# Optimization experiments

Measured on AMD Instinct MI355X. Metric: run time of the kernel, lower is better.

## Reference

```python
import jax, jax.numpy as jnp
import numpy as np

B, T, LD, HD, NH, NL = 8, 16, 256, 512, 8, 6
N = 65           # num_patches + 1 tokens per frame from encoder
AED = 64         # action_embed_dim
NDA = 11         # num_discrete_actions
MLP = 4 * HD


def _ln(x, g, b, eps=1e-5):
    m = jnp.mean(x, -1, keepdims=True)
    v = jnp.mean((x - m) ** 2, -1, keepdims=True)
    return (x - m) / jnp.sqrt(v + eps) * g + b


def setup_inputs() -> dict:
    key = jax.random.key(0)
    ks = iter(jax.random.split(key, 48))
    def nrm(shape):
        return jax.random.normal(next(ks), shape, jnp.float32) * 0.02
    inp = {
        'z_sequence': jax.random.normal(next(ks), (B, T, N, LD), jnp.float32),
        'continuous_actions': jax.random.normal(next(ks), (B, T, 2), jnp.float32),
        'discrete_actions': jax.random.randint(next(ks), (B, T), 0, NDA),
        'w_de': nrm((NDA, AED)),
        'w_cp': nrm((2, AED)), 'b_cp': jnp.zeros((AED,), jnp.float32),
        'w_ap': nrm((2 * AED, HD)), 'b_ap': jnp.zeros((HD,), jnp.float32),
        'w_tp': nrm((LD, HD)), 'b_tp': jnp.zeros((HD,), jnp.float32),
        'w_te': nrm((64, HD)),
        'ln1_g': jnp.ones((NL, HD), jnp.float32), 'ln1_b': jnp.zeros((NL, HD), jnp.float32),
        'wq': nrm((NL, HD, HD)), 'bq': jnp.zeros((NL, HD), jnp.float32),
        'wk': nrm((NL, HD, HD)), 'bk': jnp.zeros((NL, HD), jnp.float32),
        'wv': nrm((NL, HD, HD)), 'bv': jnp.zeros((NL, HD), jnp.float32),
        'wo': nrm((NL, HD, HD)), 'bo': jnp.zeros((NL, HD), jnp.float32),
        'ln2_g': jnp.ones((NL, HD), jnp.float32), 'ln2_b': jnp.zeros((NL, HD), jnp.float32),
        'w1': nrm((NL, HD, MLP)), 'b1': jnp.zeros((NL, MLP), jnp.float32),
        'w2': nrm((NL, MLP, HD)), 'b2': jnp.zeros((NL, HD), jnp.float32),
        'norm_g': jnp.ones((HD,), jnp.float32), 'norm_b': jnp.zeros((HD,), jnp.float32),
        'w_out': nrm((HD, LD)), 'b_out': jnp.zeros((LD,), jnp.float32),
        'residual_weight': jnp.float32(0.5),
    }
    return inp


def reference(z_sequence, continuous_actions, discrete_actions,
              w_de, w_cp, b_cp, w_ap, b_ap, w_tp, b_tp, w_te,
              ln1_g, ln1_b, wq, bq, wk, bk, wv, bv, wo, bo,
              ln2_g, ln2_b, w1, b1, w2, b2,
              norm_g, norm_b, w_out, b_out, residual_weight):
    Bq, Tq, Nq, Dq = z_sequence.shape
    hd = HD // NH
    scale = hd ** -0.5
    # --- per-timestep action + patch token embedding (vectorized over T) ---
    de = w_de[discrete_actions]                          # (B,T,AED)
    ce = continuous_actions @ w_cp + b_cp                # (B,T,AED)
    ac = jnp.concatenate([de, ce], -1)                   # (B,T,2*AED)
    at = (ac @ w_ap + b_ap)[:, :, None, :]               # (B,T,1,HD) action token
    pt = z_sequence @ w_tp + b_tp                        # (B,T,N,HD)
    te = w_te[:Tq][None, :, None, :]                     # (1,T,1,HD) time embedding
    x = jnp.concatenate([at + te, pt + te], axis=2)      # (B,T,1+N,HD) interleaved
    S = Tq * (Nq + 1)
    x = x.reshape(Bq, S, HD)
    # --- block-causal mask: True = cannot attend ---
    ts = jnp.repeat(jnp.arange(Tq), Nq + 1)
    mask = ts[None, :] > ts[:, None]                     # (S,S)

    def body(h, p):
        g1, be1, Wq, Bq_, Wk, Bk_, Wv, Bv_, Wo, Bo_, g2, be2, W1, B1, W2, B2 = p
        y = _ln(h, g1, be1)
        q = (y @ Wq + Bq_).reshape(Bq, S, NH, hd)
        k = (y @ Wk + Bk_).reshape(Bq, S, NH, hd)
        v = (y @ Wv + Bv_).reshape(Bq, S, NH, hd)
        sc = jnp.einsum('bqhd,bkhd->bhqk', q, k) * scale
        sc = jnp.where(mask[None, None], -jnp.inf, sc)
        a = jax.nn.softmax(sc, axis=-1)
        o = jnp.einsum('bhqk,bkhd->bqhd', a, v).reshape(Bq, S, HD)
        h = h + o @ Wo + Bo_
        y = _ln(h, g2, be2)
        h = h + jax.nn.gelu(y @ W1 + B1, approximate=False) @ W2 + B2
        return h, None

    x, _ = jax.lax.scan(body, x, (ln1_g, ln1_b, wq, bq, wk, bk, wv, bv, wo, bo,
                                  ln2_g, ln2_b, w1, b1, w2, b2))
    x = _ln(x, norm_g, norm_b)
    patch_out = x.reshape(Bq, Tq, Nq + 1, HD)[:, :, 1:, :] @ w_out + b_out
    alpha = jax.nn.sigmoid(residual_weight)
    return z_sequence + alpha * patch_out
```

## Files before the change

### kernel.cpp

```cpp
#include <hip/hip_runtime.h>
#include <hip/hip_bf16.h>
#include <cmath>

typedef __attribute__((ext_vector_type(8)))  __bf16 bf16x8;
typedef __attribute__((ext_vector_type(4)))  float  f32x4;
typedef __attribute__((ext_vector_type(16))) float  f32x16;
typedef const __attribute__((address_space(1))) void* as1cv;
typedef __attribute__((address_space(3))) void*       as3v;

static constexpr int BB = 8, TT = 16, NN = 65, LD = 256, HD = 512, NH = 8, NL = 6;
static constexpr int SS    = TT * (NN + 1);
static constexpr int ROWS  = BB * SS;
static constexpr int PROWS = BB * TT * NN;
static constexpr int MLPD  = 2048;

__global__ void transpose_cast(const float* __restrict__ in, __bf16* __restrict__ out,
                               int R, int C, size_t ibs, size_t obs)
{
  __shared__ float t[32][33];
  in  += ibs * blockIdx.z;
  out += obs * blockIdx.z;
  int bx = blockIdx.x * 32, by = blockIdx.y * 32;
  #pragma unroll
  for (int i = threadIdx.y; i < 32; i += 8)
    t[i][threadIdx.x] = in[(size_t)(by + i) * C + bx + threadIdx.x];
  __syncthreads();
  #pragma unroll
  for (int i = threadIdx.y; i < 32; i += 8)
    out[(size_t)(bx + i) * R + by + threadIdx.x] = (__bf16)t[threadIdx.x][i];
}

__global__ __launch_bounds__(256) void cast_bf16(const float* __restrict__ in,
                                                 __bf16* __restrict__ out)
{
  int i = (blockIdx.x * 256 + threadIdx.x) * 8;
  float4 a = *(const float4*)(in + i);
  float4 b = *(const float4*)(in + i + 4);
  bf16x8 o;
  o[0]=(__bf16)a.x; o[1]=(__bf16)a.y; o[2]=(__bf16)a.z; o[3]=(__bf16)a.w;
  o[4]=(__bf16)b.x; o[5]=(__bf16)b.y; o[6]=(__bf16)b.z; o[7]=(__bf16)b.w;
  *(bf16x8*)(out + i) = o;
}

__global__ void build_bqkv(const float* __restrict__ bq, const float* __restrict__ bk,
                           const float* __restrict__ bv, float* __restrict__ out)
{
  int i = blockIdx.x * 256 + threadIdx.x;
  int L = i / 1536, c = i % 1536;
  float v = (c < 512) ? bq[L*512 + c] : (c < 1024 ? bk[L*512 + c - 512] : bv[L*512 + c - 1024]);
  out[i] = v;
}

template<int FLAGS>
__global__ __launch_bounds__(256)
void gemm_bt(const __bf16* __restrict__ A, const __bf16* __restrict__ Bt,
             const float* __restrict__ bias, const float* __restrict__ resid,
             float* __restrict__ outF, __bf16* __restrict__ outB, __bf16* __restrict__ outB2,
             int M, int N, int K)
{
  __shared__ __bf16 As[64 * 64];
  __shared__ __bf16 Bs[128 * 64];
  const int tid = threadIdx.x;
  const int lane = tid & 63, w = tid >> 6;
  const int g = lane >> 4, cl = lane & 15;
  const int wr = w >> 1, wc = w & 1;
  const int gx = gridDim.x, nwg = gx * gridDim.y;
  const int orig = blockIdx.y * gx + blockIdx.x;
  const int q8 = nwg >> 3, r8 = nwg & 7;
  const int xcd = orig & 7, off = orig >> 3;
  const int tile = (xcd < r8 ? xcd * (q8 + 1) : r8 * (q8 + 1) + (xcd - r8) * q8) + off;
  const int tm = (tile / gx) * 64, tn = (tile % gx) * 128;

  f32x4 acc[2][4];
  const f32x4 zero4 = {0.f, 0.f, 0.f, 0.f};
  #pragma unroll
  for (int m = 0; m < 2; m++)
    #pragma unroll
    for (int n = 0; n < 4; n++) acc[m][n] = zero4;

  const int nk = K >> 6;
  for (int kt = 0; kt < nk; ++kt) {
    __syncthreads();
    const __bf16* Ag = A  + (size_t)tm * K + kt * 64;
    const __bf16* Bg = Bt + (size_t)tn * K + kt * 64;
    #pragma unroll
    for (int p = 0; p < 2; p++) {
      int c = p * 256 + tid;
      int row = c >> 3, j = c & 7;
      int jj = j ^ (row & 7);
      const __bf16* sa = Ag + (size_t)row * K + jj * 8;
      __builtin_amdgcn_global_load_lds((as1cv)sa, (as3v)&As[(p * 4 + w) * 512], 16, 0, 0);
    }
    #pragma unroll
    for (int p = 0; p < 4; p++) {
      int c = p * 256 + tid;
      int row = c >> 3, j = c & 7;
      int jj = j ^ (row & 7);
      const __bf16* sb = Bg + (size_t)row * K + jj * 8;
      __builtin_amdgcn_global_load_lds((as1cv)sb, (as3v)&Bs[(p * 4 + w) * 512], 16, 0, 0);
    }
    __syncthreads();
    #pragma unroll
    for (int kk = 0; kk < 2; kk++) {
      bf16x8 af[2], bfr[4];
      #pragma unroll
      for (int m = 0; m < 2; m++) {
        int row = wr * 32 + m * 16 + cl;
        af[m] = *(const bf16x8*)&As[row * 64 + ((kk * 4 + g) ^ (row & 7)) * 8];
      }
      #pragma unroll
      for (int n = 0; n < 4; n++) {
        int row = wc * 64 + n * 16 + cl;
        bfr[n] = *(const bf16x8*)&Bs[row * 64 + ((kk * 4 + g) ^ (row & 7)) * 8];
      }
      #pragma unroll
      for (int m = 0; m < 2; m++)
        #pragma unroll
        for (int n = 0; n < 4; n++)
          acc[m][n] = __builtin_amdgcn_mfma_f32_16x16x32_bf16(af[m], bfr[n], acc[m][n], 0, 0, 0);
    }
  }
  float bv[4];
  #pragma unroll
  for (int n = 0; n < 4; n++) bv[n] = bias[tn + wc * 64 + n * 16 + cl];
  #pragma unroll
  for (int m = 0; m < 2; m++) {
    int Rb = tm + wr * 32 + m * 16 + g * 4;
    #pragma unroll
    for (int i = 0; i < 4; i++) {
      int R = Rb + i;
      #pragma unroll
      for (int n = 0; n < 4; n++) {
        int C = tn + wc * 64 + n * 16 + cl;
        float v = acc[m][n][i] + bv[n];
        if (FLAGS & 1) v = 0.5f * v * (1.f + erff(v * 0.70710678118f));
        if (FLAGS & 2) v += resid[(size_t)R * N + C];
        if (FLAGS & 8) outF[(size_t)R * N + C] = v;
        if (FLAGS & 4) outB[(size_t)R * N + C] = (__bf16)v;
        if (FLAGS & 32) {
          if (C < 1024) {
            outB[(size_t)R * 1024 + C] = (__bf16)v;
          } else {
            int bb2 = R / SS, s2 = R % SS;
            int cc = C - 1024, hh = cc >> 6, dd = cc & 63;
            outB2[((size_t)((bb2 * NH + hh) * 64 + dd)) * SS + s2] = (__bf16)v;
          }
        }
      }
    }
  }
}

template<int FLAGS>
__global__ __launch_bounds__(256)
void gemm_n64(const __bf16* __restrict__ A, const __bf16* __restrict__ Bt,
              const float* __restrict__ bias, const float* __restrict__ resid,
              float* __restrict__ outF, __bf16* __restrict__ outB,
              int M, int N, int K)
{
  __shared__ __bf16 As[64 * 64];
  __shared__ __bf16 Bs[64 * 64];
  const int tid = threadIdx.x;
  const int lane = tid & 63, w = tid >> 6;
  const int g = lane >> 4, cl = lane & 15;
  const int wr = w >> 1, wc = w & 1;
  const int gx = gridDim.x, nwg = gx * gridDim.y;
  const int orig = blockIdx.y * gx + blockIdx.x;
  const int q8 = nwg >> 3, r8 = nwg & 7;
  const int xcd = orig & 7, off = orig >> 3;
  const int tile = (xcd < r8 ? xcd * (q8 + 1) : r8 * (q8 + 1) + (xcd - r8) * q8) + off;
  const int tm = (tile / gx) * 64, tn = (tile % gx) * 64;

  f32x4 acc[2][2];
  const f32x4 zero4 = {0.f, 0.f, 0.f, 0.f};
  #pragma unroll
  for (int m = 0; m < 2; m++)
    #pragma unroll
    for (int n = 0; n < 2; n++) acc[m][n] = zero4;

  const int nk = K >> 6;
  for (int kt = 0; kt < nk; ++kt) {
    __syncthreads();
    const __bf16* Ag = A  + (size_t)tm * K + kt * 64;
    const __bf16* Bg = Bt + (size_t)tn * K + kt * 64;
    #pragma unroll
    for (int p = 0; p < 2; p++) {
      int c = p * 256 + tid;
      int row = c >> 3, j = c & 7;
      int jj = j ^ (row & 7);
      const __bf16* sa = Ag + (size_t)row * K + jj * 8;
      const __bf16* sb = Bg + (size_t)row * K + jj * 8;
      __builtin_amdgcn_global_load_lds((as1cv)sa, (as3v)&As[(p * 4 + w) * 512], 16, 0, 0);
      __builtin_amdgcn_global_load_lds((as1cv)sb, (as3v)&Bs[(p * 4 + w) * 512], 16, 0, 0);
    }
    __syncthreads();
    #pragma unroll
    for (int kk = 0; kk < 2; kk++) {
      bf16x8 af[2], bfr[2];
      #pragma unroll
      for (int m = 0; m < 2; m++) {
        int row = wr * 32 + m * 16 + cl;
        af[m] = *(const bf16x8*)&As[row * 64 + ((kk * 4 + g) ^ (row & 7)) * 8];
      }
      #pragma unroll
      for (int n = 0; n < 2; n++) {
        int row = wc * 32 + n * 16 + cl;
        bfr[n] = *(const bf16x8*)&Bs[row * 64 + ((kk * 4 + g) ^ (row & 7)) * 8];
      }
      #pragma unroll
      for (int m = 0; m < 2; m++)
        #pragma unroll
        for (int n = 0; n < 2; n++)
          acc[m][n] = __builtin_amdgcn_mfma_f32_16x16x32_bf16(af[m], bfr[n], acc[m][n], 0, 0, 0);
    }
  }
  float bv[2];
  #pragma unroll
  for (int n = 0; n < 2; n++) bv[n] = bias[tn + wc * 32 + n * 16 + cl];
  #pragma unroll
  for (int m = 0; m < 2; m++) {
    int Rb = tm + wr * 32 + m * 16 + g * 4;
    #pragma unroll
    for (int i = 0; i < 4; i++) {
      int R = Rb + i;
      #pragma unroll
      for (int n = 0; n < 2; n++) {
        int C = tn + wc * 32 + n * 16 + cl;
        float v = acc[m][n][i] + bv[n];
        if (FLAGS & 1) v = 0.5f * v * (1.f + erff(v * 0.70710678118f));
        if (FLAGS & 2) v += resid[(size_t)R * N + C];
        if (FLAGS & 8) outF[(size_t)R * N + C] = v;
        if (FLAGS & 4) outB[(size_t)R * N + C] = (__bf16)v;
      }
    }
  }
}

__global__ __launch_bounds__(256) void ln_bf16(const float* __restrict__ in,
    const float* __restrict__ gam, const float* __restrict__ bet, __bf16* __restrict__ out)
{
  int w = threadIdx.x >> 6, l = threadIdx.x & 63;
  size_t row = (size_t)blockIdx.x * 4 + w;
  const float4* x4 = (const float4*)(in + row * HD);
  float4 v0 = x4[l], v1 = x4[l + 64];
  float s  = v0.x + v0.y + v0.z + v0.w + v1.x + v1.y + v1.z + v1.w;
  float q2 = v0.x*v0.x + v0.y*v0.y + v0.z*v0.z + v0.w*v0.w
           + v1.x*v1.x + v1.y*v1.y + v1.z*v1.z + v1.w*v1.w;
  #pragma unroll
  for (int m = 1; m < 64; m <<= 1) { s += __shfl_xor(s, m); q2 += __shfl_xor(q2, m); }
  float mean = s * (1.f / HD);
  float rstd = rsqrtf(q2 * (1.f / HD) - mean * mean + 1e-5f);
  int c0 = l * 4, c1 = 256 + l * 4;
  float4 g0 = *(const float4*)(gam + c0), g1 = *(const float4*)(gam + c1);
  float4 e0 = *(const float4*)(bet + c0), e1 = *(const float4*)(bet + c1);
  __bf16* o = out + row * HD;
  o[c0+0] = (__bf16)((v0.x-mean)*rstd*g0.x + e0.x);
  o[c0+1] = (__bf16)((v0.y-mean)*rstd*g0.y + e0.y);
  o[c0+2] = (__bf16)((v0.z-mean)*rstd*g0.z + e0.z);
  o[c0+3] = (__bf16)((v0.w-mean)*rstd*g0.w + e0.w);
  o[c1+0] = (__bf16)((v1.x-mean)*rstd*g1.x + e1.x);
  o[c1+1] = (__bf16)((v1.y-mean)*rstd*g1.y + e1.y);
  o[c1+2] = (__bf16)((v1.z-mean)*rstd*g1.z + e1.z);
  o[c1+3] = (__bf16)((v1.w-mean)*rstd*g1.w + e1.w);
}

__global__ __launch_bounds__(64) void act_embed(const float* __restrict__ cont,
    const int* __restrict__ disc, const float* __restrict__ w_de,
    const float* __restrict__ w_cp, const float* __restrict__ b_cp,
    const float* __restrict__ w_ap, const float* __restrict__ b_ap,
    const float* __restrict__ w_te, float* __restrict__ x)
{
  int t = blockIdx.x, b = blockIdx.y, l = threadIdx.x;
  int da = disc[b * TT + t];
  float c0 = cont[(b * TT + t) * 2], c1 = cont[(b * TT + t) * 2 + 1];
  int c = l * 8;
  float accv[8];
  #pragma unroll
  for (int j = 0; j < 8; j++) accv[j] = b_ap[c + j];
  for (int i = 0; i < 64; i++) {
    float ai = w_de[da * 64 + i];
    #pragma unroll
    for (int j = 0; j < 8; j++) accv[j] += ai * w_ap[i * HD + c + j];
  }
  for (int i = 0; i < 64; i++) {
    float ce = c0 * w_cp[i] + c1 * w_cp[64 + i] + b_cp[i];
    #pragma unroll
    for (int j = 0; j < 8; j++) accv[j] += ce * w_ap[(64 + i) * HD + c + j];
  }
  #pragma unroll
  for (int j = 0; j < 8; j++)
    x[((size_t)(b * SS) + t * 66) * HD + c + j] = accv[j] + w_te[t * HD + c + j];
}

__global__ __launch_bounds__(256) void assemble_patch(const float* __restrict__ pt,
    const float* __restrict__ te, float* __restrict__ x)
{
  int idx = (blockIdx.x * 256 + threadIdx.x) * 4;
  int c = idx & (HD - 1);
  int r = idx >> 9;
  int n = r % NN; int bt = r / NN; int t = bt & (TT - 1); int bb = bt >> 4;
  float4 v  = *(const float4*)(pt + idx);
  float4 tv = *(const float4*)(te + t * HD + c);
  v.x += tv.x; v.y += tv.y; v.z += tv.z; v.w += tv.w;
  *(float4*)(x + ((size_t)(bb * SS + t * 66 + 1 + n)) * HD + c) = v;
}

__device__ inline unsigned pkbf(float lo, float hi2) {
  unsigned short a = __builtin_bit_cast(unsigned short, (__bf16)lo);
  unsigned short b = __builtin_bit_cast(unsigned short, (__bf16)hi2);
  return (unsigned)a | ((unsigned)b << 16);
}

__global__ __launch_bounds__(256) void attn_fwd(const __bf16* __restrict__ qk,
    const __bf16* __restrict__ vT, __bf16* __restrict__ o)
{
  const int w = threadIdx.x >> 6, lane = threadIdx.x & 63;
  const int lin = (blockIdx.x & 7) * 72 + (blockIdx.x >> 3);
  const int b   = lin / 72;
  const int rem = lin % 72;
  const int h = rem / 9, j = rem % 9;
  int qt;
  if (j == 8) qt = (w == 0) ? 16 : -1;
  else        qt = (w == 0) ? j : (w == 1) ? 32 - j : (w == 2) ? 8 + j : 24 - j;
  __shared__ float red[4][32];
  if (qt < 0) return;
  const int l31 = lane & 31, hi = lane >> 5;
  const int q = qt * 32 + l31;
  const int kend = (q / 66 + 1) * 66;
  const int nkv = (((qt * 32 + 31) / 66 + 1) * 66 + 31) >> 5;

  bf16x8 qf[4];
  const __bf16* qbase = qk + (size_t)(b * SS + q) * 1024 + h * 64 + hi * 8;
  #pragma unroll
  for (int s = 0; s < 4; s++) qf[s] = *(const bf16x8*)(qbase + s * 16);

  const f32x16 z16 = {0,0,0,0,0,0,0,0,0,0,0,0,0,0,0,0};
  f32x16 accA = z16, accB = z16;
  float m = -1e30f, lsum = 0.f;

  for (int kb = 0; kb < nkv; kb++) {
    const int K0 = kb * 32;
    const __bf16* kbase = qk + (size_t)(b * SS + K0 + l31) * 1024 + 512 + h * 64 + hi * 8;
    bf16x8 kf0 = *(const bf16x8*)(kbase);
    bf16x8 kf1 = *(const bf16x8*)(kbase + 16);
    bf16x8 kf2 = *(const bf16x8*)(kbase + 32);
    bf16x8 kf3 = *(const bf16x8*)(kbase + 48);
    const __bf16* vbase = vT + (size_t)((b * NH + h) * 64 + l31) * SS + K0 + hi * 8;
    bf16x8 vf00 = *(const bf16x8*)(vbase);
    bf16x8 vf10 = *(const bf16x8*)(vbase + 16);
    bf16x8 vf01 = *(const bf16x8*)(vbase + (size_t)32 * SS);
    bf16x8 vf11 = *(const bf16x8*)(vbase + (size_t)32 * SS + 16);

    f32x16 st = z16;
    st = __builtin_amdgcn_mfma_f32_32x32x16_bf16(kf0, qf[0], st, 0, 0, 0);
    st = __builtin_amdgcn_mfma_f32_32x32x16_bf16(kf1, qf[1], st, 0, 0, 0);
    st = __builtin_amdgcn_mfma_f32_32x32x16_bf16(kf2, qf[2], st, 0, 0, 0);
    st = __builtin_amdgcn_mfma_f32_32x32x16_bf16(kf3, qf[3], st, 0, 0, 0);

    float p[16];
    #pragma unroll
    for (int r = 0; r < 16; r++) {
      int kg = K0 + (r & 3) + 8 * (r >> 2) + 4 * hi;
      p[r] = (kg < kend) ? st[r] * 0.125f : -1e30f;
    }
    float mx = fmaxf(fmaxf(fmaxf(p[0],p[1]),fmaxf(p[2],p[3])),
                     fmaxf(fmaxf(p[4],p[5]),fmaxf(p[6],p[7])));
    mx = fmaxf(mx, fmaxf(fmaxf(fmaxf(p[8],p[9]),fmaxf(p[10],p[11])),
                         fmaxf(fmaxf(p[12],p[13]),fmaxf(p[14],p[15]))));
    mx = fmaxf(mx, __shfl_xor(mx, 32));
    if (__any(mx > m + 8.f)) {
      float nm = fmaxf(m, mx);
      float alp = __expf(m - nm);
      m = nm; lsum *= alp;
      if (lane < 32) red[w][lane] = alp;
      asm volatile("s_waitcnt lgkmcnt(0)" ::: "memory");
      float4 a0 = *(const float4*)&red[w][hi * 4];
      float4 a1 = *(const float4*)&red[w][hi * 4 + 8];
      float4 a2 = *(const float4*)&red[w][hi * 4 + 16];
      float4 a3 = *(const float4*)&red[w][hi * 4 + 24];
      float afv[16] = {a0.x,a0.y,a0.z,a0.w, a1.x,a1.y,a1.z,a1.w,
                       a2.x,a2.y,a2.z,a2.w, a3.x,a3.y,a3.z,a3.w};
      #pragma unroll
      for (int r = 0; r < 16; r++) { accA[r] *= afv[r]; accB[r] *= afv[r]; }
    }
    float rs;
    #pragma unroll
    for (int r = 0; r < 16; r++) p[r] = __expf(p[r] - m);
    rs = ((p[0]+p[1])+(p[2]+p[3])) + ((p[4]+p[5])+(p[6]+p[7]))
       + ((p[8]+p[9])+(p[10]+p[11])) + ((p[12]+p[13])+(p[14]+p[15]));
    rs += __shfl_xor(rs, 32);
    lsum += rs;
    unsigned a0p = pkbf(p[0], p[1]),  a1p = pkbf(p[2], p[3]);
    unsigned a2p = pkbf(p[4], p[5]),  a3p = pkbf(p[6], p[7]);
    unsigned b0p = pkbf(p[8], p[9]),  b1p = pkbf(p[10], p[11]);
    unsigned b2p = pkbf(p[12], p[13]), b3p = pkbf(p[14], p[15]);
    unsigned s0 = __shfl_xor(a0p, 32), s1 = __shfl_xor(a1p, 32);
    unsigned s2 = __shfl_xor(a2p, 32), s3 = __shfl_xor(a3p, 32);
    unsigned t0 = __shfl_xor(b0p, 32), t1 = __shfl_xor(b1p, 32);
    unsigned t2 = __shfl_xor(b2p, 32), t3 = __shfl_xor(b3p, 32);
    union { unsigned u[4]; bf16x8 v; } af0, af1;
    af0.u[0] = hi ? s2 : a0p;  af0.u[1] = hi ? s3 : a1p;
    af0.u[2] = hi ? a2p : s0;  af0.u[3] = hi ? a3p : s1;
    af1.u[0] = hi ? t2 : b0p;  af1.u[1] = hi ? t3 : b1p;
    af1.u[2] = hi ? b2p : t0;  af1.u[3] = hi ? b3p : t1;
    accA = __builtin_amdgcn_mfma_f32_32x32x16_bf16(af0.v, vf00, accA, 0, 0, 0);
    accA = __builtin_amdgcn_mfma_f32_32x32x16_bf16(af1.v, vf10, accA, 0, 0, 0);
    accB = __builtin_amdgcn_mfma_f32_32x32x16_bf16(af0.v, vf01, accB, 0, 0, 0);
    accB = __builtin_amdgcn_mfma_f32_32x32x16_bf16(af1.v, vf11, accB, 0, 0, 0);
  }
  if (lane < 32) red[w][lane] = 1.f / lsum;
  asm volatile("s_waitcnt lgkmcnt(0)" ::: "memory");
  float4 i0 = *(const float4*)&red[w][hi * 4];
  float4 i1 = *(const float4*)&red[w][hi * 4 + 8];
  float4 i2 = *(const float4*)&red[w][hi * 4 + 16];
  float4 i3 = *(const float4*)&red[w][hi * 4 + 24];
  float iv[16] = {i0.x,i0.y,i0.z,i0.w, i1.x,i1.y,i1.z,i1.w,
                  i2.x,i2.y,i2.z,i2.w, i3.x,i3.y,i3.z,i3.w};
  __bf16* obase = o + (size_t)(b * SS + qt * 32) * HD + h * 64 + l31;
  #pragma unroll
  for (int r = 0; r < 16; r++) {
    int qrow = (r & 3) + 8 * (r >> 2) + 4 * hi;
    obase[(size_t)qrow * HD]      = (__bf16)(accA[r] * iv[r]);
    obase[(size_t)qrow * HD + 32] = (__bf16)(accB[r] * iv[r]);
  }
}

__global__ __launch_bounds__(256) void final_add(const float* __restrict__ z,
    const float* __restrict__ po, const float* __restrict__ rw, float* __restrict__ out)
{
  int idx = (blockIdx.x * 256 + threadIdx.x) * 4;
  int ld = idx & (LD - 1);
  int r = idx >> 8;
  int n = r % NN; int bt = r / NN; int t = bt & (TT - 1); int bb = bt >> 4;
  float alpha = 1.f / (1.f + __expf(-rw[0]));
  float4 zv = *(const float4*)(z + idx);
  float4 pv = *(const float4*)(po + ((size_t)(bb * SS + t * 66 + 1 + n)) * LD + ld);
  float4 ov;
  ov.x = zv.x + alpha * pv.x; ov.y = zv.y + alpha * pv.y;
  ov.z = zv.z + alpha * pv.z; ov.w = zv.w + alpha * pv.w;
  *(float4*)(out + idx) = ov;
}

extern "C" void kernel_launch(void* const* d_in, const int* in_sizes, int n_in,
                              void* d_out, int out_size, void* d_ws, size_t ws_size,
                              hipStream_t stream)
{
  const float* z    = (const float*)d_in[0];
  const float* cont = (const float*)d_in[1];
  const int*   disc = (const int*)d_in[2];
  const float* w_de = (const float*)d_in[3];
  const float* w_cp = (const float*)d_in[4];
  const float* b_cp = (const float*)d_in[5];
  const float* w_ap = (const float*)d_in[6];
  const float* b_ap = (const float*)d_in[7];
  const float* w_tp = (const float*)d_in[8];
  const float* b_tp = (const float*)d_in[9];
  const float* w_te = (const float*)d_in[10];
  const float* ln1g = (const float*)d_in[11];
  const float* ln1b = (const float*)d_in[12];
  const float* wq   = (const float*)d_in[13];
  const float* bq   = (const float*)d_in[14];
  const float* wk   = (const float*)d_in[15];
  const float* bk   = (const float*)d_in[16];
  const float* wv   = (const float*)d_in[17];
  const float* bv   = (const float*)d_in[18];
  const float* wo   = (const float*)d_in[19];
  const float* bo   = (const float*)d_in[20];
  const float* ln2g = (const float*)d_in[21];
  const float* ln2b = (const float*)d_in[22];
  const float* w1   = (const float*)d_in[23];
  const float* b1   = (const float*)d_in[24];
  const float* w2   = (const float*)d_in[25];
  const float* b2   = (const float*)d_in[26];
  const float* nog  = (const float*)d_in[27];
  const float* nob  = (const float*)d_in[28];
  const float* wout = (const float*)d_in[29];
  const float* bout = (const float*)d_in[30];
  const float* rw   = (const float*)d_in[31];
  float* out = (float*)d_out;

  char* p = (char*)d_ws;
  auto alloc = [&](size_t bytes) -> char* {
    char* r = p; p += (bytes + 255) & ~(size_t)255; return r;
  };
  __bf16* wqkvt = (__bf16*)alloc((size_t)NL * 1536 * 512 * 2);
  __bf16* wot_  = (__bf16*)alloc((size_t)NL * 512 * 512 * 2);
  __bf16* w1t   = (__bf16*)alloc((size_t)NL * 512 * 2048 * 2);
  __bf16* w2t   = (__bf16*)alloc((size_t)NL * 512 * 2048 * 2);
  __bf16* wtpt  = (__bf16*)alloc((size_t)512 * 256 * 2);
  __bf16* woutt = (__bf16*)alloc((size_t)256 * 512 * 2);
  float*  bqkv  = (float*)alloc((size_t)NL * 1536 * 4);
  __bf16* zbf   = (__bf16*)alloc((size_t)PROWS * LD * 2);
  float*  x     = (float*)alloc((size_t)ROWS * HD * 4);
  __bf16* y     = (__bf16*)alloc((size_t)ROWS * HD * 2);
  __bf16* qkb   = (__bf16*)alloc((size_t)ROWS * 1024 * 2);
  __bf16* vtb   = (__bf16*)alloc((size_t)ROWS * HD * 2);
  __bf16* ob    = (__bf16*)alloc((size_t)ROWS * HD * 2);
  __bf16* mid   = (__bf16*)alloc((size_t)ROWS * MLPD * 2);
  float*  ptb   = (float*)alloc((size_t)PROWS * HD * 4);
  (void)in_sizes; (void)n_in; (void)out_size; (void)ws_size;

  dim3 tb(32, 8);
  transpose_cast<<<dim3(16, 16, 6), tb, 0, stream>>>(wq, wqkvt,          512,  512,  262144, 786432);
  transpose_cast<<<dim3(16, 16, 6), tb, 0, stream>>>(wk, wqkvt + 262144, 512,  512,  262144, 786432);
  transpose_cast<<<dim3(16, 16, 6), tb, 0, stream>>>(wv, wqkvt + 524288, 512,  512,  262144, 786432);
  transpose_cast<<<dim3(16, 16, 6), tb, 0, stream>>>(wo, wot_,           512,  512,  262144, 262144);
  transpose_cast<<<dim3(64, 16, 6), tb, 0, stream>>>(w1, w1t,            512,  2048, 1048576, 1048576);
  transpose_cast<<<dim3(16, 64, 6), tb, 0, stream>>>(w2, w2t,            2048, 512,  1048576, 1048576);
  transpose_cast<<<dim3(16, 8, 1),  tb, 0, stream>>>(w_tp, wtpt,         256,  512,  0, 0);
  transpose_cast<<<dim3(8, 16, 1),  tb, 0, stream>>>(wout, woutt,        512,  256,  0, 0);
  build_bqkv<<<36, 256, 0, stream>>>(bq, bk, bv, bqkv);
  cast_bf16<<<(PROWS * LD) / 2048, 256, 0, stream>>>(z, zbf);

  gemm_n64<8><<<dim3(8, PROWS / 64), 256, 0, stream>>>(zbf, wtpt, b_tp, nullptr, ptb, nullptr,
                                                       PROWS, 512, 256);
  act_embed<<<dim3(16, 8), 64, 0, stream>>>(cont, disc, w_de, w_cp, b_cp, w_ap, b_ap, w_te, x);
  assemble_patch<<<(PROWS * HD) / 1024, 256, 0, stream>>>(ptb, w_te, x);

  for (int L = 0; L < NL; ++L) {
    ln_bf16<<<ROWS / 4, 256, 0, stream>>>(x, ln1g + L*HD, ln1b + L*HD, y);
    gemm_bt<32><<<dim3(12, ROWS / 64), 256, 0, stream>>>(y, wqkvt + (size_t)L*786432,
                                                         bqkv + L*1536, nullptr, nullptr,
                                                         qkb, vtb, ROWS, 1536, 512);
    attn_fwd<<<576, 256, 0, stream>>>(qkb, vtb, ob);
    gemm_n64<10><<<dim3(8, ROWS / 64), 256, 0, stream>>>(ob, wot_ + (size_t)L*262144, bo + L*HD,
                                                         x, x, nullptr, ROWS, 512, 512);
    ln_bf16<<<ROWS / 4, 256, 0, stream>>>(x, ln2g + L*HD, ln2b + L*HD, y);
    gemm_bt<5><<<dim3(16, ROWS / 64), 256, 0, stream>>>(y, w1t + (size_t)L*1048576, b1 + L*MLPD,
                                                        nullptr, nullptr, mid, nullptr,
                                                        ROWS, 2048, 512);
    gemm_n64<10><<<dim3(8, ROWS / 64), 256, 0, stream>>>(mid, w2t + (size_t)L*1048576, b2 + L*HD,
                                                         x, x, nullptr, ROWS, 512, 2048);
  }
  ln_bf16<<<ROWS / 4, 256, 0, stream>>>(x, nog, nob, y);
  gemm_n64<8><<<dim3(4, ROWS / 64), 256, 0, stream>>>(y, woutt, bout, nullptr, ptb, nullptr,
                                                      ROWS, 256, 512);
  final_add<<<(PROWS * LD) / 1024, 256, 0, stream>>>(z, ptb, rw, out);
}
```

Before: 1.068 ms.

## Split attention KV loop across warps with flash-decoding style merge

Each block now handles a single (batch, head, query-tile) and its four waves stride over the key blocks, instead of each wave taking a whole query tile with load-balanced pairing. Partial max, sum and accumulators are merged through shared memory by wave 0 with exp rescaling. This aims to raise parallelism (2112 blocks instead of 576) and shorten the critical path for long causal rows. In exchange it adds extra LDS traffic, a block barrier and a serial merge, and short tiles leave some waves with no work.

Result: faster. 1.045 ms (-2.2%).

```diff
diff --git a/kernel.cpp b/kernel.cpp
--- a/kernel.cpp
+++ b/kernel.cpp
@@ -315,20 +315,20 @@
     const __bf16* __restrict__ vT, __bf16* __restrict__ o)
 {
   const int w = threadIdx.x >> 6, lane = threadIdx.x & 63;
-  const int lin = (blockIdx.x & 7) * 72 + (blockIdx.x >> 3);
-  const int b   = lin / 72;
-  const int rem = lin % 72;
-  const int h = rem / 9, j = rem % 9;
-  int qt;
-  if (j == 8) qt = (w == 0) ? 16 : -1;
-  else        qt = (w == 0) ? j : (w == 1) ? 32 - j : (w == 2) ? 8 + j : 24 - j;
-  __shared__ float red[4][32];
-  if (qt < 0) return;
+  const int lin = (blockIdx.x & 7) * 264 + (blockIdx.x >> 3);
+  const int b   = lin / 264;
+  const int rem = lin % 264;
+  const int h = rem / 33, qt = rem % 33;
   const int l31 = lane & 31, hi = lane >> 5;
   const int q = qt * 32 + l31;
   const int kend = (q / 66 + 1) * 66;
   const int nkv = (((qt * 32 + 31) / 66 + 1) * 66 + 31) >> 5;
 
+  __shared__ float red[4][32];
+  __shared__ float lmS[4][32], llS[4][32];
+  __shared__ float laS[3][64][32];
+  __shared__ float red2[32][8];
+
   bf16x8 qf[4];
   const __bf16* qbase = qk + (size_t)(b * SS + q) * 1024 + h * 64 + hi * 8;
   #pragma unroll
@@ -338,7 +338,7 @@
   f32x16 accA = z16, accB = z16;
   float m = -1e30f, lsum = 0.f;
 
-  for (int kb = 0; kb < nkv; kb++) {
+  for (int kb = w; kb < nkv; kb += 4) {
     const int K0 = kb * 32;
     const __bf16* kbase = qk + (size_t)(b * SS + K0 + l31) * 1024 + 512 + h * 64 + hi * 8;
     bf16x8 kf0 = *(const bf16x8*)(kbase);
@@ -408,20 +408,40 @@
     accB = __builtin_amdgcn_mfma_f32_32x32x16_bf16(af0.v, vf01, accB, 0, 0, 0);
     accB = __builtin_amdgcn_mfma_f32_32x32x16_bf16(af1.v, vf11, accB, 0, 0, 0);
   }
-  if (lane < 32) red[w][lane] = 1.f / lsum;
+
+  if (lane < 32) { lmS[w][lane] = m; llS[w][lane] = lsum; }
+  if (w > 0) {
+    #pragma unroll
+    for (int r = 0; r < 16; r++) {
+      laS[w - 1][lane][r]      = accA[r];
+      laS[w - 1][lane][16 + r] = accB[r];
+    }
+  }
+  __syncthreads();
+  if (w != 0) return;
+  float m0 = lmS[0][l31], m1 = lmS[1][l31], m2 = lmS[2][l31], m3 = lmS[3][l31];
+  float M = fmaxf(fmaxf(m0, m1), fmaxf(m2, m3));
+  float f0 = __expf(m0 - M), f1 = __expf(m1 - M);
+  float f2 = __expf(m2 - M), f3 = __expf(m3 - M);
+  float L = llS[0][l31] * f0 + llS[1][l31] * f1 + llS[2][l31] * f2 + llS[3][l31] * f3;
+  if (lane < 32) {
+    red2[lane][0] = f0; red2[lane][1] = f1;
+    red2[lane][2] = f2; red2[lane][3] = f3;
+    red2[lane][4] = 1.f / L;
+  }
   asm volatile("s_waitcnt lgkmcnt(0)" ::: "memory");
-  float4 i0 = *(const float4*)&red[w][hi * 4];
-  float4 i1 = *(const float4*)&red[w][hi * 4 + 8];
-  float4 i2 = *(const float4*)&red[w][hi * 4 + 16];
-  float4 i3 = *(const float4*)&red[w][hi * 4 + 24];
-  float iv[16] = {i0.x,i0.y,i0.z,i0.w, i1.x,i1.y,i1.z,i1.w,
-                  i2.x,i2.y,i2.z,i2.w, i3.x,i3.y,i3.z,i3.w};
   __bf16* obase = o + (size_t)(b * SS + qt * 32) * HD + h * 64 + l31;
   #pragma unroll
   for (int r = 0; r < 16; r++) {
-    int qrow = (r & 3) + 8 * (r >> 2) + 4 * hi;
-    obase[(size_t)qrow * HD]      = (__bf16)(accA[r] * iv[r]);
-    obase[(size_t)qrow * HD + 32] = (__bf16)(accB[r] * iv[r]);
+    int qr = (r & 3) + 8 * (r >> 2) + 4 * hi;
+    float4 fv = *(const float4*)&red2[qr][0];
+    float il = red2[qr][4];
+    float oa = (accA[r] * fv.x + laS[0][lane][r] * fv.y
+              + laS[1][lane][r] * fv.z + laS[2][lane][r] * fv.w) * il;
+    float ob = (accB[r] * fv.x + laS[0][lane][16 + r] * fv.y
+              + laS[1][lane][16 + r] * fv.z + laS[2][lane][16 + r] * fv.w) * il;
+    obase[(size_t)qr * HD]      = (__bf16)oa;
+    obase[(size_t)qr * HD + 32] = (__bf16)ob;
   }
 }
 
@@ -522,7 +542,7 @@
     gemm_bt<32><<<dim3(12, ROWS / 64), 256, 0, stream>>>(y, wqkvt + (size_t)L*786432,
                                                          bqkv + L*1536, nullptr, nullptr,
                                                          qkb, vtb, ROWS, 1536, 512);
-    attn_fwd<<<576, 256, 0, stream>>>(qkb, vtb, ob);
+    attn_fwd<<<2112, 256, 0, stream>>>(qkb, vtb, ob);
     gemm_n64<10><<<dim3(8, ROWS / 64), 256, 0, stream>>>(ob, wot_ + (size_t)L*262144, bo + L*HD,
                                                          x, x, nullptr, ROWS, 512, 512);
     ln_bf16<<<ROWS / 4, 256, 0, stream>>>(x, ln2g + L*HD, ln2b + L*HD, y);
```
